# Kernel optimization log

Measured on AMD Instinct MI355X. Metric: run time of the kernel, lower is better.

The kernel has to match this reference:

```python
import jax, jax.numpy as jnp
import numpy as np


def quantize_uniform(x, n_bits, clip):
    # clamp to [-clip, clip], round to 2^(1-n_bits)*clip grid, cap at clip*(1-b)
    b = 2.0 ** (1 - n_bits)
    xc = jnp.clip(x, -clip, clip)
    return clip * jnp.minimum(b * jnp.round(xc / (b * clip)), 1.0 - b)


def quantize_act(x, n_bits, clip):
    # clip to [0, clip], round to 2^-n_bits grid, cap at 1 - 2^-n_bits
    s = 2.0 ** n_bits
    xc = jnp.clip(x, 0.0, clip)
    return jnp.minimum(jnp.round(xc * s) / s, 1.0 - 1.0 / s)


def qconv(x, w, b, pad):
    # fake-quantized conv: weights/bias quant(8,1), input quant(8,4), output quant(8,8)
    wq = quantize_uniform(w, 8, 1.0)
    bq = quantize_uniform(b, 8, 1.0)
    xq = quantize_uniform(x, 8, 4.0)
    y = jax.lax.conv_general_dilated(
        xq, wq, window_strides=(1, 1), padding=[(pad, pad), (pad, pad)],
        dimension_numbers=('NCHW', 'OIHW', 'NCHW'))
    y = y + bq[None, :, None, None]
    return quantize_uniform(y, 8, 8.0)


def setup_inputs() -> dict:
    key = jax.random.key(0)
    ks = jax.random.split(key, 7)
    N, Cin, H, W = 32, 128, 56, 56
    Sq, E1, E3 = 32, 128, 128
    x = jax.random.normal(ks[0], (N, Cin, H, W), dtype=jnp.float32)
    w_sq = jax.random.normal(ks[1], (Sq, Cin, 1, 1), dtype=jnp.float32) * 0.05
    b_sq = jax.random.normal(ks[2], (Sq,), dtype=jnp.float32) * 0.05
    w_e1 = jax.random.normal(ks[3], (E1, Sq, 1, 1), dtype=jnp.float32) * 0.05
    b_e1 = jax.random.normal(ks[4], (E1,), dtype=jnp.float32) * 0.05
    w_e3 = jax.random.normal(ks[5], (E3, Sq, 3, 3), dtype=jnp.float32) * 0.05
    b_e3 = jax.random.normal(ks[6], (E3,), dtype=jnp.float32) * 0.05
    return {'x': x, 'w_sq': w_sq, 'b_sq': b_sq, 'w_e1': w_e1, 'b_e1': b_e1,
            'w_e3': w_e3, 'b_e3': b_e3}


def reference(x, w_sq, b_sq, w_e1, b_e1, w_e3, b_e3):
    h = jax.nn.relu(qconv(x, w_sq, b_sq, pad=0))
    h = quantize_act(h, 13, 4.0)
    y1 = jax.nn.relu(qconv(h, w_e1, b_e1, pad=0))
    y3 = jax.nn.relu(qconv(h, w_e3, b_e3, pad=1))
    return jnp.concatenate([y1, y3], axis=1)
```

## Files before the change

### kernel.cpp

```cpp
#include <hip/hip_runtime.h>
#include <stdint.h>

typedef __bf16 bf16x8 __attribute__((ext_vector_type(8)));
typedef float  f32x4  __attribute__((ext_vector_type(4)));

#define HW   3136
#define WID  56
#define CIN  128
#define SQ   32

#define OFF_BSQ 0
#define OFF_BE  32
#define WSQF_BYTES_OFF 1152
#define WE1F_BYTES_OFF 9344
#define WE3F_BYTES_OFF 17536

__device__ __forceinline__ float quant_w8(float x){
  float xc = fminf(fmaxf(x,-1.f),1.f);
  return fminf(rintf(xc*128.f)*0.0078125f, 0.9921875f);
}
__device__ __forceinline__ ushort wq_int_bf16(float x){
  float xc = fminf(fmaxf(x,-1.f),1.f);
  float n = fminf(rintf(xc*128.f), 127.f);
  return (ushort)(__float_as_uint(n)>>16);
}
__device__ __forceinline__ uint pack2f(float a, float b){
  return (__float_as_uint(a)>>16) | (__float_as_uint(b)&0xffff0000u);
}

__global__ void prep_kernel(const float* __restrict__ wsq, const float* __restrict__ bsq,
                            const float* __restrict__ we1, const float* __restrict__ be1,
                            const float* __restrict__ we3, const float* __restrict__ be3,
                            float* __restrict__ ws){
  int tid = blockIdx.x*blockDim.x+threadIdx.x;
  int nth = gridDim.x*blockDim.x;
  ushort* wsqf = (ushort*)((char*)ws + WSQF_BYTES_OFF);
  ushort* we1f = (ushort*)((char*)ws + WE1F_BYTES_OFF);
  ushort* we3f = (ushort*)((char*)ws + WE3F_BYTES_OFF);
  for (int i=tid;i<SQ;i+=nth) ws[OFF_BSQ+i]=quant_w8(bsq[i]);
  for (int i=tid;i<256;i+=nth) ws[OFF_BE+i] = (i<128)? quant_w8(be1[i]) : quant_w8(be3[i-128]);
  for (int i=tid;i<4096;i+=nth){
    int mfkc=i>>9, l=(i>>3)&63, j=i&7;
    int mf=mfkc>>2, kc=mfkc&3;
    int co=mf*16+(l&15), ci=kc*32+(l>>4)*8+j;
    wsqf[i] = wq_int_bf16(wsq[co*CIN+ci]);
  }
  for (int i=tid;i<4096;i+=nth){
    int mf=i>>9, l=(i>>3)&63, j=i&7;
    int co=mf*16+(l&15), ci=(l>>4)*8+j;
    we1f[i] = wq_int_bf16(we1[co*SQ+ci]);
  }
  for (int i=tid;i<36864;i+=nth){
    int mf=i/4608, r=i-mf*4608, t=r>>9, l=(r>>3)&63, j=r&7;
    int co=mf*16+(l&15), ci=(l>>4)*8+j;
    we3f[i] = wq_int_bf16(we3[(co*SQ+ci)*9+t]);
  }
}

__global__ __launch_bounds__(512, 2) void fire_kernel(const float* __restrict__ x,
    const float* __restrict__ ws, float* __restrict__ out){
  __shared__ uint4 lds4[2320];
  int wg = blockIdx.x;
  int logical = (wg & 7)*32 + (wg >> 3);
  int n   = logical >> 3;
  int bry = logical & 7;
  int tid = threadIdx.x, w = tid>>6, lane = tid&63;
  int colg = lane&15, kg = lane>>4;
  int R0 = bry*7;
  int vr0 = (R0==0) ? 0 : R0-1;
  int vr1 = (R0+7 > 55) ? 55 : R0+7;
  int limit = (vr1+1)*WID;
  int nblk = ((vr1-vr0+1)*WID + 15)>>4;
  int base_px = vr0*WID;

  uint4 z = make_uint4(0,0,0,0);
  for (int i=tid; i<2320; i+=512) lds4[i] = z;
  __syncthreads();

  {
    const bf16x8* wsqf = (const bf16x8*)((const char*)ws + WSQF_BYTES_OFF);
    bf16x8 W[8];
    #pragma unroll
    for (int q=0;q<8;++q) W[q] = wsqf[q*64 + lane];
    float bias[2][4];
    #pragma unroll
    for (int mf=0;mf<2;++mf)
      #pragma unroll
      for (int r=0;r<4;++r) bias[mf][r] = ws[OFF_BSQ + mf*16 + kg*4 + r];

    for (int b=w; b<nblk; b+=8){
      int px = base_px + b*16 + colg;
      int pxc = (px < limit) ? px : (limit-1);
      const float* xp = x + (size_t)n*CIN*HW + pxc;
      float xv[32];
      #pragma unroll
      for (int kc=0;kc<4;++kc)
        #pragma unroll
        for (int j=0;j<8;++j)
          xv[kc*8+j] = xp[(size_t)(kc*32 + kg*8 + j)*HW];

      bf16x8 Bf[4];
      #pragma unroll
      for (int kc=0;kc<4;++kc){
        float m[8];
        #pragma unroll
        for (int j=0;j<8;++j){
          float v = fminf(fmaxf(xv[kc*8+j],-4.f),4.f);
          m[j] = fminf(rintf(v*32.f), 127.f);
        }
        union { uint u[4]; bf16x8 v; } cv;
        #pragma unroll
        for (int q=0;q<4;++q) cv.u[q] = pack2f(m[q*2], m[q*2+1]);
        Bf[kc] = cv.v;
      }

      f32x4 acc0 = (f32x4){0.f,0.f,0.f,0.f};
      f32x4 acc1 = (f32x4){0.f,0.f,0.f,0.f};
      #pragma unroll
      for (int kc=0;kc<4;++kc){
        acc0 = __builtin_amdgcn_mfma_f32_16x16x32_bf16(W[kc],   Bf[kc], acc0, 0,0,0);
        acc1 = __builtin_amdgcn_mfma_f32_16x16x32_bf16(W[4+kc], Bf[kc], acc1, 0,0,0);
      }

      if (px < limit){
        int rr = px/WID, c = px - rr*WID;
        int ph = (rr - R0 + 1)*58 + c + 1;
        #pragma unroll
        for (int mf=0;mf<2;++mf){
          f32x4 a = mf ? acc1 : acc0;
          float m[4];
          #pragma unroll
          for (int r=0;r<4;++r){
            float y = fmaf(a[r], 0.000244140625f, bias[mf][r]);
            y = fminf(fmaxf(y,-8.f),8.f);
            y = fminf(rintf(y*16.f)*0.0625f, 7.9375f);
            y = fmaxf(y,0.f);
            y = fminf(y,4.f);
            y = fminf(y,0.9998779296875f);
            m[r] = rintf(y*32.f);
          }
          int chunk = mf*2 + (kg>>1);
          int idx = ph*4 + (chunk ^ ((ph>>1)&3));
          uint* dst = (uint*)&lds4[idx] + (kg&1)*2;
          dst[0] = pack2f(m[0], m[1]);
          dst[1] = pack2f(m[2], m[3]);
        }
      }
    }
  }
  __syncthreads();

  int wid = w&3, rpl = w>>2;
  const bf16x8* we1f = (const bf16x8*)((const char*)ws + WE1F_BYTES_OFF);
  const bf16x8* we3f = (const bf16x8*)((const char*)ws + WE3F_BYTES_OFF);
  const bf16x8* lbase = (const bf16x8*)lds4;

  #pragma unroll
  for (int s=0; s<2; ++s){
    int rp = rpl*2 + s;
    int baseh[7];
    #pragma unroll
    for (int nf=0;nf<7;++nf){
      int p = rp*112 + nf*16 + colg;
      int rr = p/WID, c = p - rr*WID;
      baseh[nf] = (rr+1)*58 + c + 1;
    }

    f32x4 acc[4][7];
    #pragma unroll
    for (int mi=0;mi<4;++mi)
      #pragma unroll
      for (int nf=0;nf<7;++nf)
        acc[mi][nf] = (f32x4){0.f,0.f,0.f,0.f};

    #pragma unroll
    for (int t=0;t<9;++t){
      int off = (t/3 - 1)*58 + (t%3 - 1);
      bf16x8 B[7];
      #pragma unroll
      for (int nf=0;nf<7;++nf){
        int ph = baseh[nf] + off;
        int idx = ph*4 + (kg ^ ((ph>>1)&3));
        B[nf] = lbase[idx];
      }
      bf16x8 A2 = we3f[(wid*9+t)*64 + lane];
      bf16x8 A3 = we3f[((wid+4)*9+t)*64 + lane];
      #pragma unroll
      for (int nf=0;nf<7;++nf){
        acc[2][nf] = __builtin_amdgcn_mfma_f32_16x16x32_bf16(B[nf], A2, acc[2][nf], 0,0,0);
        acc[3][nf] = __builtin_amdgcn_mfma_f32_16x16x32_bf16(B[nf], A3, acc[3][nf], 0,0,0);
      }
      if (t==4){
        bf16x8 A0 = we1f[wid*64 + lane];
        bf16x8 A1 = we1f[(wid+4)*64 + lane];
        #pragma unroll
        for (int nf=0;nf<7;++nf){
          acc[0][nf] = __builtin_amdgcn_mfma_f32_16x16x32_bf16(B[nf], A0, acc[0][nf], 0,0,0);
          acc[1][nf] = __builtin_amdgcn_mfma_f32_16x16x32_bf16(B[nf], A1, acc[1][nf], 0,0,0);
        }
      }
    }

    #pragma unroll
    for (int mi=0;mi<4;++mi){
      int co = (wid+mi*4)*16 + colg;
      float bias = ws[OFF_BE + co];
      float* opb = out + (size_t)(n*256+co)*HW + R0*WID + rp*112 + kg*4;
      #pragma unroll
      for (int nf=0;nf<7;++nf){
        if (rp == 3 && (nf*16 + kg*4) >= 56) continue;
        f32x4 a = acc[mi][nf];
        f32x4 yv;
        #pragma unroll
        for (int r=0;r<4;++r){
          float y = fmaf(a[r], 0.000244140625f, bias);
          y = fminf(fmaxf(y,-8.f),8.f);
          y = fminf(rintf(y*16.f)*0.0625f, 7.9375f);
          y = fmaxf(y,0.f);
          yv[r] = y;
        }
        *(f32x4*)(opb + nf*16) = yv;
      }
    }
  }
}

extern "C" void kernel_launch(void* const* d_in, const int* in_sizes, int n_in,
                              void* d_out, int out_size, void* d_ws, size_t ws_size,
                              hipStream_t stream){
  const float* x   = (const float*)d_in[0];
  const float* wsq = (const float*)d_in[1];
  const float* bsq = (const float*)d_in[2];
  const float* we1 = (const float*)d_in[3];
  const float* be1 = (const float*)d_in[4];
  const float* we3 = (const float*)d_in[5];
  const float* be3 = (const float*)d_in[6];
  float* out = (float*)d_out;
  float* ws  = (float*)d_ws;

  hipLaunchKernelGGL(prep_kernel, dim3(64), dim3(256), 0, stream,
                     wsq, bsq, we1, be1, we3, be3, ws);
  hipLaunchKernelGGL(fire_kernel, dim3(256), dim3(512), 0, stream, x, ws, out);
}
```

Measured before the change: 43.82 us.

## Stage expand-conv outputs through LDS for coalesced global stores

The expand phase is reorganised so each wave owns a single 16-channel output block and loops over all four row-pairs, instead of two row-pairs with four channel blocks. Accumulators are transposed through a new shared-memory staging buffer, so each lane writes 16-byte chunks along the pixel dimension, giving long contiguous runs per channel in the dominant output write. This costs an extra ~58KB of LDS, several block-wide barriers per row-pair, and repeated LDS fragment reads of the squeeze activations. The launch bound's minimum-blocks hint is dropped, relaxing the register limit.

Measured after the change: 44.60 us. No clear change (+1.8%).

```diff
diff --git a/kernel.cpp b/kernel.cpp
--- a/kernel.cpp
+++ b/kernel.cpp
@@ -26,6 +26,12 @@
 }
 __device__ __forceinline__ uint pack2f(float a, float b){
   return (__float_as_uint(a)>>16) | (__float_as_uint(b)&0xffff0000u);
+}
+__device__ __forceinline__ float eplg(float a, float bias){
+  float y = fmaf(a, 0.000244140625f, bias);
+  y = fminf(fmaxf(y,-8.f),8.f);
+  y = fminf(rintf(y*16.f)*0.0625f, 7.9375f);
+  return fmaxf(y,0.f);
 }
 
 __global__ void prep_kernel(const float* __restrict__ wsq, const float* __restrict__ bsq,
@@ -57,9 +63,10 @@
   }
 }
 
-__global__ __launch_bounds__(512, 2) void fire_kernel(const float* __restrict__ x,
+__global__ __launch_bounds__(512) void fire_kernel(const float* __restrict__ x,
     const float* __restrict__ ws, float* __restrict__ out){
   __shared__ uint4 lds4[2320];
+  __shared__ float stage[128*115];
   int wg = blockIdx.x;
   int logical = (wg & 7)*32 + (wg >> 3);
   int n   = logical >> 3;
@@ -82,11 +89,11 @@
     bf16x8 W[8];
     #pragma unroll
     for (int q=0;q<8;++q) W[q] = wsqf[q*64 + lane];
-    float bias[2][4];
+    float sbias[2][4];
     #pragma unroll
     for (int mf=0;mf<2;++mf)
       #pragma unroll
-      for (int r=0;r<4;++r) bias[mf][r] = ws[OFF_BSQ + mf*16 + kg*4 + r];
+      for (int r=0;r<4;++r) sbias[mf][r] = ws[OFF_BSQ + mf*16 + kg*4 + r];
 
     for (int b=w; b<nblk; b+=8){
       int px = base_px + b*16 + colg;
@@ -131,7 +138,7 @@
           float m[4];
           #pragma unroll
           for (int r=0;r<4;++r){
-            float y = fmaf(a[r], 0.000244140625f, bias[mf][r]);
+            float y = fmaf(a[r], 0.000244140625f, sbias[mf][r]);
             y = fminf(fmaxf(y,-8.f),8.f);
             y = fminf(rintf(y*16.f)*0.0625f, 7.9375f);
             y = fmaxf(y,0.f);
@@ -150,14 +157,16 @@
   }
   __syncthreads();
 
-  int wid = w&3, rpl = w>>2;
   const bf16x8* we1f = (const bf16x8*)((const char*)ws + WE1F_BYTES_OFF);
   const bf16x8* we3f = (const bf16x8*)((const char*)ws + WE3F_BYTES_OFF);
   const bf16x8* lbase = (const bf16x8*)lds4;
-
-  #pragma unroll
-  for (int s=0; s<2; ++s){
-    int rp = rpl*2 + s;
+  int lsub = lane & 31, lpl = lane >> 5;
+
+  for (int rp=0;rp<4;++rp){
+    int npx = (rp==3) ? 56 : 112;
+    bool act = (lsub < 28) && (lsub*4 < npx);
+    size_t obase = (size_t)(n*256)*HW + R0*WID + rp*112 + lsub*4;
+
     int baseh[7];
     #pragma unroll
     for (int nf=0;nf<7;++nf){
@@ -166,61 +175,61 @@
       baseh[nf] = (rr+1)*58 + c + 1;
     }
 
-    f32x4 acc[4][7];
-    #pragma unroll
-    for (int mi=0;mi<4;++mi)
-      #pragma unroll
-      for (int nf=0;nf<7;++nf)
-        acc[mi][nf] = (f32x4){0.f,0.f,0.f,0.f};
-
+    f32x4 acc1[7];
+    {
+      bf16x8 A0 = we1f[w*64 + lane];
+      #pragma unroll
+      for (int nf=0;nf<7;++nf){
+        int ph = baseh[nf];
+        int idx = ph*4 + (kg ^ ((ph>>1)&3));
+        acc1[nf] = __builtin_amdgcn_mfma_f32_16x16x32_bf16(lbase[idx], A0,
+                     (f32x4){0.f,0.f,0.f,0.f}, 0,0,0);
+      }
+    }
+    __syncthreads();
+    #pragma unroll
+    for (int nf=0;nf<7;++nf)
+      *(f32x4*)&stage[(w*16+colg)*115 + nf*16 + kg*4] = acc1[nf];
+    __syncthreads();
+    #pragma unroll
+    for (int q=0;q<8;++q){
+      int p = w*16 + q*2 + lpl;
+      float bias = ws[OFF_BE + p];
+      f32x4 a = *(const f32x4*)&stage[p*115 + lsub*4];
+      f32x4 yv;
+      #pragma unroll
+      for (int r=0;r<4;++r) yv[r] = eplg(a[r], bias);
+      if (act) *(f32x4*)(out + obase + (size_t)p*HW) = yv;
+    }
+
+    f32x4 acc3[7];
+    #pragma unroll
+    for (int nf=0;nf<7;++nf) acc3[nf] = (f32x4){0.f,0.f,0.f,0.f};
     #pragma unroll
     for (int t=0;t<9;++t){
       int off = (t/3 - 1)*58 + (t%3 - 1);
-      bf16x8 B[7];
+      bf16x8 A = we3f[(w*9+t)*64 + lane];
       #pragma unroll
       for (int nf=0;nf<7;++nf){
         int ph = baseh[nf] + off;
         int idx = ph*4 + (kg ^ ((ph>>1)&3));
-        B[nf] = lbase[idx];
-      }
-      bf16x8 A2 = we3f[(wid*9+t)*64 + lane];
-      bf16x8 A3 = we3f[((wid+4)*9+t)*64 + lane];
-      #pragma unroll
-      for (int nf=0;nf<7;++nf){
-        acc[2][nf] = __builtin_amdgcn_mfma_f32_16x16x32_bf16(B[nf], A2, acc[2][nf], 0,0,0);
-        acc[3][nf] = __builtin_amdgcn_mfma_f32_16x16x32_bf16(B[nf], A3, acc[3][nf], 0,0,0);
-      }
-      if (t==4){
-        bf16x8 A0 = we1f[wid*64 + lane];
-        bf16x8 A1 = we1f[(wid+4)*64 + lane];
-        #pragma unroll
-        for (int nf=0;nf<7;++nf){
-          acc[0][nf] = __builtin_amdgcn_mfma_f32_16x16x32_bf16(B[nf], A0, acc[0][nf], 0,0,0);
-          acc[1][nf] = __builtin_amdgcn_mfma_f32_16x16x32_bf16(B[nf], A1, acc[1][nf], 0,0,0);
-        }
-      }
-    }
-
-    #pragma unroll
-    for (int mi=0;mi<4;++mi){
-      int co = (wid+mi*4)*16 + colg;
-      float bias = ws[OFF_BE + co];
-      float* opb = out + (size_t)(n*256+co)*HW + R0*WID + rp*112 + kg*4;
-      #pragma unroll
-      for (int nf=0;nf<7;++nf){
-        if (rp == 3 && (nf*16 + kg*4) >= 56) continue;
-        f32x4 a = acc[mi][nf];
-        f32x4 yv;
-        #pragma unroll
-        for (int r=0;r<4;++r){
-          float y = fmaf(a[r], 0.000244140625f, bias);
-          y = fminf(fmaxf(y,-8.f),8.f);
-          y = fminf(rintf(y*16.f)*0.0625f, 7.9375f);
-          y = fmaxf(y,0.f);
-          yv[r] = y;
-        }
-        *(f32x4*)(opb + nf*16) = yv;
-      }
+        acc3[nf] = __builtin_amdgcn_mfma_f32_16x16x32_bf16(lbase[idx], A, acc3[nf], 0,0,0);
+      }
+    }
+    __syncthreads();
+    #pragma unroll
+    for (int nf=0;nf<7;++nf)
+      *(f32x4*)&stage[(w*16+colg)*115 + nf*16 + kg*4] = acc3[nf];
+    __syncthreads();
+    #pragma unroll
+    for (int q=0;q<8;++q){
+      int p = w*16 + q*2 + lpl;
+      float bias = ws[OFF_BE + 128 + p];
+      f32x4 a = *(const f32x4*)&stage[p*115 + lsub*4];
+      f32x4 yv;
+      #pragma unroll
+      for (int r=0;r<4;++r) yv[r] = eplg(a[r], bias);
+      if (act) *(f32x4*)(out + obase + (size_t)(128+p)*HW) = yv;
     }
   }
 }
```
